# Kernel optimization log

Hardware: AMD Instinct MI355X
Metric: run time of the kernel (lower is better)

Reference implementation:

```python
import jax, jax.numpy as jnp
import numpy as np

B, T, E, H = 1024, 200, 128, 128
N_ITEMS, N_CATS = 100000, 1000
LN_EPS = 1e-5


def _prelu(x, a):
    return jnp.where(x >= 0, x, a * x)


def _layernorm(x, g, b):
    m = x.mean(-1, keepdims=True)
    v = ((x - m) ** 2).mean(-1, keepdims=True)
    return (x - m) / jnp.sqrt(v + LN_EPS) * g + b


def setup_inputs() -> dict:
    key = jax.random.key(0)
    it = iter(jax.random.split(key, 64))
    nx = lambda: next(it)
    def lin(out_d, in_d):
        s = 1.0 / np.sqrt(in_d)
        return jax.random.uniform(nx(), (out_d, in_d), jnp.float32, -s, s)
    inp = {}
    inp['behavior_ids'] = jax.random.randint(nx(), (B, T), 0, N_ITEMS)
    inp['candidate_id'] = jax.random.randint(nx(), (B,), 0, N_ITEMS)
    inp['candidate_cat'] = jax.random.randint(nx(), (B,), 0, N_CATS)
    inp['dense_features'] = jax.random.normal(nx(), (B, 5), jnp.float32)
    inp['item_emb'] = (jax.random.normal(nx(), (N_ITEMS, E), jnp.float32) * 0.01).at[0].set(0.0)
    inp['cat_emb'] = (jax.random.normal(nx(), (N_CATS, E // 2), jnp.float32) * 0.01).at[0].set(0.0)
    # nn.GRU params (gate order r,z,n)
    inp['gru_wih'] = lin(3 * H, E)
    inp['gru_whh'] = lin(3 * H, H)
    inp['gru_bih'] = jnp.zeros((3 * H,), jnp.float32)
    inp['gru_bhh'] = jnp.zeros((3 * H,), jnp.float32)
    # auxiliary_net: Linear(H,E) -> ReLU -> Linear(E,1)
    inp['aux_w1'] = lin(E, H); inp['aux_b1'] = jnp.zeros((E,), jnp.float32)
    inp['aux_w2'] = lin(1, E); inp['aux_b2'] = jnp.zeros((1,), jnp.float32)
    # attention_mlp: Linear(3H,64) -> PReLU -> Linear(64,1)
    inp['att_w1'] = lin(64, 3 * H); inp['att_b1'] = jnp.zeros((64,), jnp.float32)
    inp['att_a'] = jnp.array(0.25, jnp.float32)
    inp['att_w2'] = lin(1, 64); inp['att_b2'] = jnp.zeros((1,), jnp.float32)
    # AUGRU gates: Linear(2H, H) each
    inp['wz'] = lin(H, 2 * H); inp['bz'] = jnp.zeros((H,), jnp.float32)
    inp['wr'] = lin(H, 2 * H); inp['br'] = jnp.zeros((H,), jnp.float32)
    inp['wh'] = lin(H, 2 * H); inp['bh'] = jnp.zeros((H,), jnp.float32)
    # dense_proj Linear(5,32)
    inp['dp_w'] = lin(32, 5); inp['dp_b'] = jnp.zeros((32,), jnp.float32)
    # MLP: 352 -> 256 -> 128 -> 64, each Linear + LayerNorm + PReLU
    dims = [H + E + E // 2 + 32, 256, 128, 64]
    for i in range(3):
        inp[f'm_w{i+1}'] = lin(dims[i + 1], dims[i])
        inp[f'm_b{i+1}'] = jnp.zeros((dims[i + 1],), jnp.float32)
        inp[f'ln_g{i+1}'] = jnp.ones((dims[i + 1],), jnp.float32)
        inp[f'ln_b{i+1}'] = jnp.zeros((dims[i + 1],), jnp.float32)
        inp[f'pa{i+1}'] = jnp.array(0.25, jnp.float32)
    # 3 task heads Linear(64,1), stacked
    inp['heads_w'] = lin(3, 64); inp['heads_b'] = jnp.zeros((3,), jnp.float32)
    return inp


def _forward_core(behavior_ids, candidate_id, candidate_cat, dense_features,
                  item_emb, cat_emb, gru_wih, gru_whh, gru_bih, gru_bhh,
                  aux_w1, aux_b1, aux_w2, aux_b2,
                  att_w1, att_b1, att_a, att_w2, att_b2,
                  wz, bz, wr, br, wh, bh, dp_w, dp_b,
                  m_w1, m_b1, ln_g1, ln_b1, pa1,
                  m_w2, m_b2, ln_g2, ln_b2, pa2,
                  m_w3, m_b3, ln_g3, ln_b3, pa3,
                  heads_w, heads_b):
    beh = item_emb[behavior_ids]            # [B,T,E]
    cand = item_emb[candidate_id]           # [B,E]
    catv = cat_emb[candidate_cat]           # [B,E//2]
    Bsz = beh.shape[0]
    Hd = gru_whh.shape[1]
    h0 = jnp.zeros((Bsz, Hd), beh.dtype)
    # --- interest extractor GRU (cuDNN GRU math, gate order r,z,n) ---
    xp = jnp.einsum('bte,ge->btg', beh, gru_wih) + gru_bih  # [B,T,3H]
    def gru_step(h, x):
        hp = h @ gru_whh.T + gru_bhh
        xr, xz, xn = jnp.split(x, 3, -1)
        hr, hz, hn = jnp.split(hp, 3, -1)
        r = jax.nn.sigmoid(xr + hr)
        z = jax.nn.sigmoid(xz + hz)
        n = jnp.tanh(xn + r * hn)
        hnew = (1 - z) * n + z * h
        return hnew, hnew
    _, hs = jax.lax.scan(gru_step, h0, jnp.swapaxes(xp, 0, 1))
    hs = jnp.swapaxes(hs, 0, 1)             # [B,T,H]
    # --- auxiliary logits ---
    aux = jax.nn.relu(hs[:, :-1] @ aux_w1.T + aux_b1) @ aux_w2.T + aux_b2  # [B,T-1,1]
    # --- attention (embed_dim == hidden_size so cand_proj == candidate_emb) ---
    ce = cand[:, None, :]
    att_in = jnp.concatenate([hs, jnp.broadcast_to(ce, hs.shape), hs * ce], -1)  # [B,T,3H]
    scores = (_prelu(att_in @ att_w1.T + att_b1, att_a) @ att_w2.T + att_b2)[..., 0]
    att = jax.nn.softmax(scores, axis=-1)   # [B,T]
    # --- AUGRU: attention-modulated update gate ---
    def augru_step(h, xs):
        x, a = xs                           # x: [B,H], a: [B]
        comb = jnp.concatenate([x, h], -1)
        z = jax.nn.sigmoid(comb @ wz.T + bz)
        r = jax.nn.sigmoid(comb @ wr.T + br)
        comb_r = jnp.concatenate([x, r * h], -1)
        ht = jnp.tanh(comb_r @ wh.T + bh)
        zp = a[:, None] * z
        return (1 - zp) * h + zp * ht, None
    hT, _ = jax.lax.scan(augru_step, h0, (jnp.swapaxes(hs, 0, 1), att.T))
    # --- fusion MLP (dropout is identity in eval) ---
    dense_out = dense_features @ dp_w.T + dp_b
    x = jnp.concatenate([hT, cand, catv, dense_out], -1)  # [B,352]
    for (w, b, g, be, a) in ((m_w1, m_b1, ln_g1, ln_b1, pa1),
                             (m_w2, m_b2, ln_g2, ln_b2, pa2),
                             (m_w3, m_b3, ln_g3, ln_b3, pa3)):
        x = _prelu(_layernorm(x @ w.T + b, g, be), a)
    preds = jax.nn.sigmoid(x @ heads_w.T + heads_b)  # [B,3] == 3 heads of [B,1]
    return preds, aux


def reference(behavior_ids, candidate_id, candidate_cat, dense_features,
              item_emb, cat_emb, gru_wih, gru_whh, gru_bih, gru_bhh,
              aux_w1, aux_b1, aux_w2, aux_b2,
              att_w1, att_b1, att_a, att_w2, att_b2,
              wz, bz, wr, br, wh, bh, dp_w, dp_b,
              m_w1, m_b1, ln_g1, ln_b1, pa1,
              m_w2, m_b2, ln_g2, ln_b2, pa2,
              m_w3, m_b3, ln_g3, ln_b3, pa3,
              heads_w, heads_b):
    return _forward_core(behavior_ids, candidate_id, candidate_cat, dense_features,
                         item_emb, cat_emb, gru_wih, gru_whh, gru_bih, gru_bhh,
                         aux_w1, aux_b1, aux_w2, aux_b2,
                         att_w1, att_b1, att_a, att_w2, att_b2,
                         wz, bz, wr, br, wh, bh, dp_w, dp_b,
                         m_w1, m_b1, ln_g1, ln_b1, pa1,
                         m_w2, m_b2, ln_g2, ln_b2, pa2,
                         m_w3, m_b3, ln_g3, ln_b3, pa3,
                         heads_w, heads_b)
```

## Files before the change

kernel.cpp:

```cpp
#include <hip/hip_runtime.h>


typedef __bf16 bf16;
typedef float f32x4 __attribute__((ext_vector_type(4)));
typedef __bf16 bf16x8 __attribute__((ext_vector_type(8)));
typedef __bf16 bf16x4 __attribute__((ext_vector_type(4)));

#define MFMA16(a, b, c) __builtin_amdgcn_mfma_f32_16x16x32_bf16((a), (b), (c), 0, 0, 0)

#define BATCH 1024
#define SEQT 200
#define F32_ONE 0x3F800000u

__device__ __forceinline__ float sigm(float x) {
  return __builtin_amdgcn_rcpf(1.0f + __expf(-x));
}
__device__ __forceinline__ float tanh_fast(float x) {
  float ax = fabsf(x);
  float t = 1.0f - 2.0f * __builtin_amdgcn_rcpf(__expf(2.0f * ax) + 1.0f);
  return copysignf(t, x);
}

__device__ __forceinline__ void bar_lgkm() {
  asm volatile("s_waitcnt lgkmcnt(0)\n\ts_barrier" ::: "memory");
}

__device__ __forceinline__ void dma16(const void* g, void* l) {
  __builtin_amdgcn_global_load_lds((__attribute__((address_space(1))) void*)g,
                                   (__attribute__((address_space(3))) void*)l,
                                   16, 0, 0);
}

template <typename DT> __device__ __forceinline__ float ldf(const DT* p, long i);
template <> __device__ __forceinline__ float ldf<bf16>(const bf16* p, long i) { return (float)p[i]; }
template <> __device__ __forceinline__ float ldf<float>(const float* p, long i) { return p[i]; }

template <typename DT> __device__ __forceinline__ bf16x8 ld8(const DT* p, long i);
template <> __device__ __forceinline__ bf16x8 ld8<bf16>(const bf16* p, long i) {
  return *(const bf16x8*)(p + i);
}
template <> __device__ __forceinline__ bf16x8 ld8<float>(const float* p, long i) {
  f32x4 a = *(const f32x4*)(p + i);
  f32x4 b = *(const f32x4*)(p + i + 4);
  bf16x8 r;
  r[0] = (bf16)a[0]; r[1] = (bf16)a[1]; r[2] = (bf16)a[2]; r[3] = (bf16)a[3];
  r[4] = (bf16)b[0]; r[5] = (bf16)b[1]; r[6] = (bf16)b[2]; r[7] = (bf16)b[3];
  return r;
}

template <typename DT>
__device__ __forceinline__ void cast_body(const DT* __restrict__ src, bf16* __restrict__ dst) {
  const long i = ((long)blockIdx.x * 256 + threadIdx.x) * 8;
  if (i < 100000L * 128) *(bf16x8*)(dst + i) = ld8(src, i);
}
__global__ __launch_bounds__(256) void k_cast(
    const unsigned* __restrict__ disc, const void* src, bf16* dst) {
  if (*disc == F32_ONE) cast_body<float>((const float*)src, dst);
  else                  cast_body<bf16>((const bf16*)src, dst);
}

template <typename DT>
__device__ __forceinline__ void prep_body(
    const int* __restrict__ cid, const int* __restrict__ ccat,
    const DT* __restrict__ dense, const DT* __restrict__ item_emb,
    const DT* __restrict__ cat_emb, const DT* __restrict__ dp_w,
    const DT* __restrict__ dp_b, bf16* __restrict__ candbuf, bf16* __restrict__ xf) {
  const int b = blockIdx.x;
  const int t = threadIdx.x;
  bf16 v = (bf16)ldf(item_emb, (long)cid[b] * 128 + t);
  candbuf[b * 128 + t] = v;
  xf[(long)b * 352 + 128 + t] = v;
  if (t < 64) xf[(long)b * 352 + 256 + t] = (bf16)ldf(cat_emb, (long)ccat[b] * 64 + t);
  if (t < 32) {
    float s = ldf(dp_b, t);
    for (int k = 0; k < 5; k++) s += ldf(dense, b * 5 + k) * ldf(dp_w, t * 5 + k);
    xf[(long)b * 352 + 320 + t] = (bf16)s;
  }
}
__global__ __launch_bounds__(128) void k_prep(
    const unsigned* __restrict__ disc, const int* cid, const int* ccat,
    const void* dense, const void* item_emb, const void* cat_emb,
    const void* dp_w, const void* dp_b, bf16* candbuf, bf16* xf) {
  if (*disc == F32_ONE)
    prep_body<float>(cid, ccat, (const float*)dense, (const float*)item_emb,
                     (const float*)cat_emb, (const float*)dp_w, (const float*)dp_b, candbuf, xf);
  else
    prep_body<bf16>(cid, ccat, (const bf16*)dense, (const bf16*)item_emb,
                    (const bf16*)cat_emb, (const bf16*)dp_w, (const bf16*)dp_b, candbuf, xf);
}

template <typename DT>
__device__ __forceinline__ void gru5_body(
    const int* __restrict__ ids, const bf16* __restrict__ ieb,
    const DT* __restrict__ wih, const DT* __restrict__ whh,
    const DT* __restrict__ bih, const DT* __restrict__ bhh, bf16* __restrict__ hs,
    bf16 (*hA)[16][136], bf16 (*xb)[4][16][128]) {
  const int b0 = blockIdx.x * 16;
  const int tid = threadIdx.x;
  const int w = tid >> 6, lane = tid & 63, l15 = lane & 15, quad = lane >> 4;
  const int nc = w * 16 + l15;

  for (int i = tid; i < 2 * 16 * 136; i += 512) ((bf16*)hA)[i] = (bf16)0.0f;

  bf16x8 wir[4], wiz[4], win_[4], whr[4], whz[4], whn[4];
#pragma unroll
  for (int k = 0; k < 4; k++) {
    const long off = k * 32 + quad * 8;
    wir[k] = ld8(wih, (long)nc * 128 + off);
    wiz[k] = ld8(wih, (long)(128 + nc) * 128 + off);
    win_[k] = ld8(wih, (long)(256 + nc) * 128 + off);
    whr[k] = ld8(whh, (long)nc * 128 + off);
    whz[k] = ld8(whh, (long)(128 + nc) * 128 + off);
    whn[k] = ld8(whh, (long)(256 + nc) * 128 + off);
  }
  const float br_s = ldf(bih, nc) + ldf(bhh, nc);
  const float bz_s = ldf(bih, 128 + nc) + ldf(bhh, 128 + nc);
  const float bxn_s = ldf(bih, 256 + nc);
  const float bhn_s = ldf(bhh, 256 + nc);

  const int idrow = (tid >> 4) & 15;
  const int* idbase = ids + (long)(b0 + idrow) * SEQT;
  const int srcoff = ((tid & 15) ^ (idrow & 7)) * 8;

  auto DMA = [&](const int4 id4, int buf) {
#pragma unroll
    for (int j = 0; j < 2; j++) {
      const int slot = j * 2 + (tid >> 8);
      dma16(ieb + (long)((&id4.x)[slot]) * 128 + srcoff,
            (char*)&xb[buf][0][0][0] + (j * 512 + tid) * 16);
    }
  };

  const int srow = tid >> 5, sch = (tid & 31) * 4;
  bf16* hsb = hs + ((long)(b0 + srow) * SEQT) * 128 + sch;

  float hreg[4] = {0.f, 0.f, 0.f, 0.f};
  const f32x4 z4 = {0.f, 0.f, 0.f, 0.f};

  int4 idv = *(const int4*)(idbase);
  DMA(idv, 0);
  idv = *(const int4*)(idbase + 4);
  asm volatile("s_waitcnt vmcnt(1)" ::: "memory");
  __builtin_amdgcn_sched_barrier(0);
  __builtin_amdgcn_s_barrier();

#define GRU_STEP(P, S, WAITC)                                                  \
  {                                                                            \
    const int tt = t0 + (S);                                                   \
    bf16x8 af[4], xaf[4];                                                      \
    _Pragma("unroll") for (int k = 0; k < 4; k++) {                            \
      af[k] = *(const bf16x8*)&hA[P][l15][k * 32 + quad * 8];                  \
      xaf[k] = *(const bf16x8*)((const char*)&xb[buf][S][0][0] + l15 * 256 +   \
                                ((((k << 2) + quad) ^ (l15 & 7)) << 4));       \
    }                                                                          \
    { const int slot = tt ? tt - 1 : 0;                                        \
      bf16x4 hv = *(const bf16x4*)&hA[P][srow][sch];                           \
      *(bf16x4*)(hsb + (long)slot * 128) = hv; }                               \
    f32x4 ar = z4, az = z4, axn = z4, ahn = z4;                                \
    _Pragma("unroll") for (int k = 0; k < 4; k++) {                            \
      ar = MFMA16(xaf[k], wir[k], ar);                                         \
      az = MFMA16(xaf[k], wiz[k], az);                                         \
      axn = MFMA16(xaf[k], win_[k], axn);                                      \
    }                                                                          \
    _Pragma("unroll") for (int k = 0; k < 4; k++) {                            \
      ar = MFMA16(af[k], whr[k], ar);                                          \
      az = MFMA16(af[k], whz[k], az);                                          \
      ahn = MFMA16(af[k], whn[k], ahn);                                        \
    }                                                                          \
    _Pragma("unroll") for (int r = 0; r < 4; r++) {                            \
      float r_ = sigm(ar[r] + br_s);                                           \
      float z_ = sigm(az[r] + bz_s);                                           \
      float n_ = tanh_fast(axn[r] + bxn_s + r_ * (ahn[r] + bhn_s));            \
      float hnew = (1.0f - z_) * n_ + z_ * hreg[r];                            \
      hreg[r] = hnew;                                                          \
      hA[(P) ^ 1][quad * 4 + r][nc] = (bf16)hnew;                              \
    }                                                                          \
    if (WAITC) {                                                               \
       \
      asm volatile("s_waitcnt vmcnt(5) lgkmcnt(0)\n\ts_barrier" ::: "memory"); \
    } else {                                                                   \
      bar_lgkm();                                                              \
    }                                                                          \
  }

  for (int c = 0; c < 50; c++) {
    const int t0 = c * 4;
    const int buf = c & 1;
    if (c < 49) {
      DMA(idv, buf ^ 1);
      int nid = (c + 2) * 4; if (nid > 196) nid = 196;
      idv = *(const int4*)(idbase + nid);
    }
    GRU_STEP(0, 0, 0) GRU_STEP(1, 1, 0) GRU_STEP(0, 2, 0) GRU_STEP(1, 3, (c < 49))
  }
#undef GRU_STEP
  { bf16x4 hv = *(const bf16x4*)&hA[0][srow][sch];
    *(bf16x4*)(hsb + (long)(SEQT - 1) * 128) = hv; }
}
__global__ __launch_bounds__(512, 1) void k_gru5(
    const unsigned* __restrict__ disc, const int* ids, const bf16* ieb,
    const void* wih, const void* whh, const void* bih, const void* bhh, bf16* hs) {
  __shared__ __align__(16) bf16 hA[2][16][136];
  __shared__ __align__(16) bf16 xb[2][4][16][128];
  if (*disc == F32_ONE)
    gru5_body<float>(ids, ieb, (const float*)wih, (const float*)whh,
                     (const float*)bih, (const float*)bhh, hs, hA, xb);
  else
    gru5_body<bf16>(ids, ieb, (const bf16*)wih, (const bf16*)whh,
                    (const bf16*)bih, (const bf16*)bhh, hs, hA, xb);
}

template <typename DT>
__device__ __forceinline__ void attaux_body(
    const bf16* __restrict__ hs, const int* __restrict__ cid,
    const DT* __restrict__ item_emb,
    const DT* __restrict__ aw1, const DT* __restrict__ ab1,
    const DT* __restrict__ aw2, const DT* __restrict__ ab2,
    const DT* __restrict__ tw1, const DT* __restrict__ tb1, const DT* __restrict__ ta,
    const DT* __restrict__ tw2, const DT* __restrict__ tb2,
    float* __restrict__ sc, float* __restrict__ outaux,
    bf16 (*As)[64][128], float (*scPt)[64], float (*scPa)[64]) {
  const int t0 = blockIdx.x * 64;
  const int b0 = blockIdx.y * 16;
  const int tid = threadIdx.x, w = tid >> 6, lane = tid & 63, l15 = lane & 15, quad = lane >> 4;

  const int tn = w * 16 + l15;
  bf16x8 wth[4], wtc[4], wthc[4], wa0[4], wa1[4];
#pragma unroll
  for (int k = 0; k < 4; k++) {
    const long off = k * 32 + quad * 8;
    wth[k]  = ld8(tw1, (long)tn * 384 + off);
    wtc[k]  = ld8(tw1, (long)tn * 384 + 128 + off);
    wthc[k] = ld8(tw1, (long)tn * 384 + 256 + off);
    wa0[k]  = ld8(aw1, (long)((2 * w) * 16 + l15) * 128 + off);
    wa1[k]  = ld8(aw1, (long)((2 * w + 1) * 16 + l15) * 128 + off);
  }
  const float tb1c = ldf(tb1, tn), tw2c = ldf(tw2, tn);
  const float ab1c0 = ldf(ab1, (2 * w) * 16 + l15), aw2c0 = ldf(aw2, (2 * w) * 16 + l15);
  const float ab1c1 = ldf(ab1, (2 * w + 1) * 16 + l15), aw2c1 = ldf(aw2, (2 * w + 1) * 16 + l15);
  const float aP = ldf(ta, 0), tb2s = ldf(tb2, 0), ab2s = ldf(ab2, 0);

  auto DMA = [&](int b, int buf) {
#pragma unroll
    for (int c = 0; c < 4; c++) {
      const int idx = c * 256 + tid;
      const int row = idx >> 4, p = idx & 15;
      int t = t0 + row; if (t > SEQT - 1) t = SEQT - 1;
      const bf16* src = hs + ((long)b * SEQT + t) * 128 + ((p ^ (row & 7)) * 8);
      dma16(src, (char*)(&As[buf][0][0]) + idx * 16);
    }
  };
  auto CANDLD = [&](int b, bf16x8* cf) {
#pragma unroll
    for (int k = 0; k < 4; k++)
      cf[k] = ld8(item_emb, (long)cid[b] * 128 + k * 32 + quad * 8);
  };

  const f32x4 z4 = {0.f, 0.f, 0.f, 0.f};
  bf16x8 candA[4], candB[4];
  DMA(b0, 0);
  CANDLD(b0, candA);
  asm volatile("s_waitcnt vmcnt(0)" ::: "memory");
  __builtin_amdgcn_sched_barrier(0);
  __builtin_amdgcn_s_barrier();

#define AA_STEP(BI, CUSE, CPF)                                                 \
  {                                                                            \
    const int b = b0 + (BI);                                                   \
    const int buf = (BI) & 1;                                                  \
    if ((BI) + 1 < 16) { DMA(b + 1, buf ^ 1); CANDLD(b + 1, CPF); }            \
    _Pragma("unroll") for (int m = 0; m < 4; m++) {                            \
      const bf16* arow = &As[buf][m * 16 + l15][0];                            \
      bf16x8 af[4], hcf[4];                                                    \
      _Pragma("unroll") for (int k = 0; k < 4; k++)                            \
        af[k] = *(const bf16x8*)((const char*)arow +                           \
                                 (((k * 4 + quad) ^ (l15 & 7)) << 4));         \
      _Pragma("unroll") for (int k = 0; k < 4; k++)                            \
      _Pragma("unroll") for (int j = 0; j < 8; j++)                            \
        hcf[k][j] = (bf16)((float)af[k][j] * (float)CUSE[k][j]);               \
      f32x4 at = z4, aa0 = z4, aa1 = z4;                                       \
      _Pragma("unroll") for (int k = 0; k < 4; k++) {                          \
        at = MFMA16(af[k], wth[k], at);                                        \
        at = MFMA16(CUSE[k], wtc[k], at);                                      \
        at = MFMA16(hcf[k], wthc[k], at);                                      \
        aa0 = MFMA16(af[k], wa0[k], aa0);                                      \
        aa1 = MFMA16(af[k], wa1[k], aa1);                                      \
      }                                                                        \
      float tp[4], ap[4];                                                      \
      _Pragma("unroll") for (int r = 0; r < 4; r++) {                          \
        float y = at[r] + tb1c;                                                \
        y = (y >= 0.f) ? y : aP * y;                                           \
        tp[r] = y * tw2c;                                                      \
        float y0 = aa0[r] + ab1c0;                                             \
        float y1 = aa1[r] + ab1c1;                                             \
        ap[r] = (y0 > 0.f ? y0 : 0.f) * aw2c0 + (y1 > 0.f ? y1 : 0.f) * aw2c1; \
      }                                                                        \
      _Pragma("unroll") for (int mm = 1; mm < 16; mm <<= 1)                    \
      _Pragma("unroll") for (int r = 0; r < 4; r++) {                          \
        tp[r] += __shfl_xor(tp[r], mm, 64);                                    \
        ap[r] += __shfl_xor(ap[r], mm, 64);                                    \
      }                                                                        \
      if (l15 == 0) {                                                          \
        *(float4*)&scPt[w][m * 16 + quad * 4] =                                \
            make_float4(tp[0], tp[1], tp[2], tp[3]);                           \
        *(float4*)&scPa[w][m * 16 + quad * 4] =                                \
            make_float4(ap[0], ap[1], ap[2], ap[3]);                           \
      }                                                                        \
    }                                                                          \
    bar_lgkm();                                                                \
    if (tid < 64) {                                                            \
      int t = t0 + tid;                                                        \
      if (t < SEQT) {                                                          \
        float s = scPt[0][tid] + scPt[1][tid] + scPt[2][tid] + scPt[3][tid];   \
        sc[(long)b * SEQT + t] = s + tb2s;                                     \
      }                                                                        \
    } else if (tid < 128) {                                                    \
      int tt2 = tid - 64, t = t0 + tt2;                                        \
      if (t < SEQT - 1) {                                                      \
        float s = scPa[0][tt2] + scPa[1][tt2] + scPa[2][tt2] + scPa[3][tt2];   \
        outaux[(long)b * 199 + t] = s + ab2s;                                  \
      }                                                                        \
    }                                                                          \
    asm volatile("s_waitcnt vmcnt(0) lgkmcnt(0)" ::: "memory");                \
    __builtin_amdgcn_sched_barrier(0);                                         \
    __builtin_amdgcn_s_barrier();                                              \
  }

  for (int bi = 0; bi < 16; bi += 2) {
    AA_STEP(bi, candA, candB)
    AA_STEP(bi + 1, candB, candA)
  }
#undef AA_STEP
}
__global__ __launch_bounds__(256, 1) void k_attaux(
    const unsigned* __restrict__ disc, const bf16* hs, const int* cid,
    const void* item_emb,
    const void* aw1, const void* ab1, const void* aw2, const void* ab2,
    const void* tw1, const void* tb1, const void* ta, const void* tw2, const void* tb2,
    float* sc, float* outaux) {
  __shared__ __align__(16) bf16 As[2][64][128];
  __shared__ __align__(16) float scPt[4][64];
  __shared__ __align__(16) float scPa[4][64];
  if (*disc == F32_ONE)
    attaux_body<float>(hs, cid, (const float*)item_emb,
                       (const float*)aw1, (const float*)ab1, (const float*)aw2, (const float*)ab2,
                       (const float*)tw1, (const float*)tb1, (const float*)ta,
                       (const float*)tw2, (const float*)tb2, sc, outaux, As, scPt, scPa);
  else
    attaux_body<bf16>(hs, cid, (const bf16*)item_emb,
                      (const bf16*)aw1, (const bf16*)ab1, (const bf16*)aw2, (const bf16*)ab2,
                      (const bf16*)tw1, (const bf16*)tb1, (const bf16*)ta,
                      (const bf16*)tw2, (const bf16*)tb2, sc, outaux, As, scPt, scPa);
}

__global__ __launch_bounds__(256) void k_softmax(float* __restrict__ sc) {
  const int b = blockIdx.x, tid = threadIdx.x;
  __shared__ float red[256];
  float v = (tid < SEQT) ? sc[(long)b * SEQT + tid] : -1e30f;
  red[tid] = v; __syncthreads();
  for (int s = 128; s > 0; s >>= 1) { if (tid < s) red[tid] = fmaxf(red[tid], red[tid + s]); __syncthreads(); }
  float mx = red[0]; __syncthreads();
  float e = (tid < SEQT) ? __expf(v - mx) : 0.f;
  red[tid] = e; __syncthreads();
  for (int s = 128; s > 0; s >>= 1) { if (tid < s) red[tid] += red[tid + s]; __syncthreads(); }
  float inv = 1.0f / red[0];
  if (tid < SEQT) sc[(long)b * SEQT + tid] = e * inv;
}

template <typename DT>
__device__ __forceinline__ void augru5_body(
    const bf16* __restrict__ hsrc, const float* __restrict__ att,
    const DT* __restrict__ wz, const DT* __restrict__ wr, const DT* __restrict__ wh,
    const DT* __restrict__ bzv, const DT* __restrict__ brv, const DT* __restrict__ bhv,
    bf16* __restrict__ xf_out,
    bf16 (*hA)[16][136], bf16 (*rhA)[136], float (*attL)[201],
    bf16 (*xb)[4][16][128]) {
  const int b0 = blockIdx.x * 16;
  const int tid = threadIdx.x;
  const int w = tid >> 6, lane = tid & 63, l15 = lane & 15, quad = lane >> 4;
  const int nc = w * 16 + l15;

  for (int i = tid; i < 2 * 16 * 136; i += 512) ((bf16*)hA)[i] = (bf16)0.0f;
  for (int i = tid; i < 16 * SEQT; i += 512) {
    int r = i / SEQT, c = i - r * SEQT;
    attL[r][c] = att[(long)(b0 + r) * SEQT + c];
  }

  bf16x8 wzx[4], wzh[4], wrx[4], wrh[4], whx[4], whh_[4];
#pragma unroll
  for (int k = 0; k < 4; k++) {
    const long off = k * 32 + quad * 8;
    wzx[k] = ld8(wz, (long)nc * 256 + off);
    wzh[k] = ld8(wz, (long)nc * 256 + 128 + off);
    wrx[k] = ld8(wr, (long)nc * 256 + off);
    wrh[k] = ld8(wr, (long)nc * 256 + 128 + off);
    whx[k] = ld8(wh, (long)nc * 256 + off);
    whh_[k] = ld8(wh, (long)nc * 256 + 128 + off);
  }
  const float bz_s = ldf(bzv, nc);
  const float br_s = ldf(brv, nc);
  const float bh_s = ldf(bhv, nc);

  const int drow = (tid >> 4) & 15;
  const int srcoff = ((tid & 15) ^ (drow & 7)) * 8;
  auto DMA = [&](int t0, int buf) {
#pragma unroll
    for (int j = 0; j < 2; j++) {
      const int slot = j * 2 + (tid >> 8);
      dma16(hsrc + ((long)(b0 + drow) * SEQT + t0 + slot) * 128 + srcoff,
            (char*)&xb[buf][0][0][0] + (j * 512 + tid) * 16);
    }
  };

  float hreg[4] = {0.f, 0.f, 0.f, 0.f};
  const f32x4 z4 = {0.f, 0.f, 0.f, 0.f};

  DMA(0, 0);
  asm volatile("s_waitcnt vmcnt(0)" ::: "memory");
  __builtin_amdgcn_sched_barrier(0);
  __builtin_amdgcn_s_barrier();

#define AUGRU_STEP(P, S, WAITC)                                                \
  {                                                                            \
    const int tt = t0 + (S);                                                   \
    bf16x8 af[4], xaf[4];                                                      \
    _Pragma("unroll") for (int k = 0; k < 4; k++) {                            \
      af[k] = *(const bf16x8*)&hA[P][l15][k * 32 + quad * 8];                  \
      xaf[k] = *(const bf16x8*)((const char*)&xb[buf][S][0][0] + l15 * 256 +   \
                                ((((k << 2) + quad) ^ (l15 & 7)) << 4));       \
    }                                                                          \
    f32x4 az = z4, ar = z4, axh = z4;                                          \
    _Pragma("unroll") for (int k = 0; k < 4; k++) {                            \
      az = MFMA16(xaf[k], wzx[k], az);                                         \
      ar = MFMA16(xaf[k], wrx[k], ar);                                         \
      axh = MFMA16(xaf[k], whx[k], axh);                                       \
    }                                                                          \
    _Pragma("unroll") for (int k = 0; k < 4; k++) {                            \
      az = MFMA16(af[k], wzh[k], az);                                          \
      ar = MFMA16(af[k], wrh[k], ar);                                          \
    }                                                                          \
    float zp[4];                                                               \
    _Pragma("unroll") for (int r = 0; r < 4; r++) {                            \
      float a_ = attL[quad * 4 + r][tt];                                       \
      float z_ = sigm(az[r] + bz_s);                                           \
      float r_ = sigm(ar[r] + br_s);                                           \
      zp[r] = a_ * z_;                                                         \
      rhA[quad * 4 + r][nc] = (bf16)(r_ * hreg[r]);                            \
    }                                                                          \
    bar_lgkm();                                                                \
    bf16x8 rf[4];                                                              \
    _Pragma("unroll") for (int k = 0; k < 4; k++)                              \
      rf[k] = *(const bf16x8*)&rhA[l15][k * 32 + quad * 8];                    \
    f32x4 ahh = axh;                                                           \
    _Pragma("unroll") for (int k = 0; k < 4; k++)                              \
      ahh = MFMA16(rf[k], whh_[k], ahh);                                       \
    _Pragma("unroll") for (int r = 0; r < 4; r++) {                            \
      float ht = tanh_fast(ahh[r] + bh_s);                                     \
      float hnew = (1.f - zp[r]) * hreg[r] + zp[r] * ht;                       \
      hreg[r] = hnew;                                                          \
      hA[(P) ^ 1][quad * 4 + r][nc] = (bf16)hnew;                              \
    }                                                                          \
    if (WAITC) {                                                               \
                     \
      asm volatile("s_waitcnt vmcnt(0) lgkmcnt(0)\n\ts_barrier" ::: "memory"); \
    } else {                                                                   \
      bar_lgkm();                                                              \
    }                                                                          \
  }

  for (int c = 0; c < 50; c++) {
    const int t0 = c * 4;
    const int buf = c & 1;
    if (c < 49) DMA((c + 1) * 4, buf ^ 1);
    AUGRU_STEP(0, 0, 0) AUGRU_STEP(1, 1, 0) AUGRU_STEP(0, 2, 0) AUGRU_STEP(1, 3, (c < 49))
  }
#undef AUGRU_STEP
#pragma unroll
  for (int r = 0; r < 4; r++)
    xf_out[(long)(b0 + quad * 4 + r) * 352 + nc] = (bf16)hreg[r];
}
__global__ __launch_bounds__(512, 1) void k_augru5(
    const unsigned* __restrict__ disc, const bf16* hsrc, const float* att,
    const void* wz, const void* wr, const void* wh,
    const void* bzv, const void* brv, const void* bhv, bf16* xf_out) {
  __shared__ __align__(16) bf16 hA[2][16][136];
  __shared__ __align__(16) bf16 rhA[16][136];
  __shared__ __align__(16) float attL[16][201];
  __shared__ __align__(16) bf16 xb[2][4][16][128];
  if (*disc == F32_ONE)
    augru5_body<float>(hsrc, att, (const float*)wz, (const float*)wr, (const float*)wh,
                       (const float*)bzv, (const float*)brv, (const float*)bhv, xf_out,
                       hA, rhA, attL, xb);
  else
    augru5_body<bf16>(hsrc, att, (const bf16*)wz, (const bf16*)wr, (const bf16*)wh,
                      (const bf16*)bzv, (const bf16*)brv, (const bf16*)bhv, xf_out,
                      hA, rhA, attL, xb);
}

template <typename DT>
__device__ __forceinline__ void mlp_body(
    const bf16* __restrict__ xf,
    const DT* __restrict__ w1, const DT* __restrict__ b1, const DT* __restrict__ g1, const DT* __restrict__ be1, const DT* __restrict__ pa1,
    const DT* __restrict__ w2, const DT* __restrict__ b2, const DT* __restrict__ g2, const DT* __restrict__ be2, const DT* __restrict__ pa2,
    const DT* __restrict__ w3, const DT* __restrict__ b3, const DT* __restrict__ g3, const DT* __restrict__ be3, const DT* __restrict__ pa3,
    const DT* __restrict__ hw, const DT* __restrict__ hb, float* __restrict__ preds,
    float (*xs)[352], float (*ys)[256]) {
  const int tid = threadIdx.x, w = tid >> 6, lane = tid & 63;
  const int b = blockIdx.x * 4 + w;
  for (int i = lane; i < 352; i += 64) xs[w][i] = (float)xf[(long)b * 352 + i];
  __syncthreads();
  float acc1[4];
#pragma unroll
  for (int oi = 0; oi < 4; oi++) {
    int o = lane + 64 * oi;
    float s = ldf(b1, o);
    for (int k = 0; k < 352; k += 8) {
      bf16x8 wv = ld8(w1, (long)o * 352 + k);
#pragma unroll
      for (int j = 0; j < 8; j++) s += xs[w][k + j] * (float)wv[j];
    }
    acc1[oi] = s;
  }
  float sm = acc1[0] + acc1[1] + acc1[2] + acc1[3];
#pragma unroll
  for (int m = 1; m < 64; m <<= 1) sm += __shfl_xor(sm, m, 64);
  float mean = sm * (1.0f / 256.0f);
  float vs = 0.f;
#pragma unroll
  for (int oi = 0; oi < 4; oi++) { float d = acc1[oi] - mean; vs += d * d; }
#pragma unroll
  for (int m = 1; m < 64; m <<= 1) vs += __shfl_xor(vs, m, 64);
  float rstd = rsqrtf(vs * (1.0f / 256.0f) + 1e-5f);
  float a1 = ldf(pa1, 0);
#pragma unroll
  for (int oi = 0; oi < 4; oi++) {
    int o = lane + 64 * oi;
    float y = (acc1[oi] - mean) * rstd * ldf(g1, o) + ldf(be1, o);
    ys[w][o] = (y >= 0.f) ? y : a1 * y;
  }
  __syncthreads();
  float acc2[2];
#pragma unroll
  for (int oi = 0; oi < 2; oi++) {
    int o = lane + 64 * oi;
    float s = ldf(b2, o);
    for (int k = 0; k < 256; k += 8) {
      bf16x8 wv = ld8(w2, (long)o * 256 + k);
#pragma unroll
      for (int j = 0; j < 8; j++) s += ys[w][k + j] * (float)wv[j];
    }
    acc2[oi] = s;
  }
  sm = acc2[0] + acc2[1];
#pragma unroll
  for (int m = 1; m < 64; m <<= 1) sm += __shfl_xor(sm, m, 64);
  mean = sm * (1.0f / 128.0f);
  vs = 0.f;
#pragma unroll
  for (int oi = 0; oi < 2; oi++) { float d = acc2[oi] - mean; vs += d * d; }
#pragma unroll
  for (int m = 1; m < 64; m <<= 1) vs += __shfl_xor(vs, m, 64);
  rstd = rsqrtf(vs * (1.0f / 128.0f) + 1e-5f);
  float a2 = ldf(pa2, 0);
  __syncthreads();
#pragma unroll
  for (int oi = 0; oi < 2; oi++) {
    int o = lane + 64 * oi;
    float y = (acc2[oi] - mean) * rstd * ldf(g2, o) + ldf(be2, o);
    xs[w][o] = (y >= 0.f) ? y : a2 * y;
  }
  __syncthreads();
  float s3 = ldf(b3, lane);
  for (int k = 0; k < 128; k += 8) {
    bf16x8 wv = ld8(w3, (long)lane * 128 + k);
#pragma unroll
    for (int j = 0; j < 8; j++) s3 += xs[w][k + j] * (float)wv[j];
  }
  sm = s3;
#pragma unroll
  for (int m = 1; m < 64; m <<= 1) sm += __shfl_xor(sm, m, 64);
  mean = sm * (1.0f / 64.0f);
  float d3 = s3 - mean;
  vs = d3 * d3;
#pragma unroll
  for (int m = 1; m < 64; m <<= 1) vs += __shfl_xor(vs, m, 64);
  rstd = rsqrtf(vs * (1.0f / 64.0f) + 1e-5f);
  float a3 = ldf(pa3, 0);
  float y3 = d3 * rstd * ldf(g3, lane) + ldf(be3, lane);
  y3 = (y3 >= 0.f) ? y3 : a3 * y3;
  ys[w][lane] = y3;
  __syncthreads();
  if (lane < 3) {
    float s = ldf(hb, lane);
    for (int k = 0; k < 64; k++) s += ys[w][k] * ldf(hw, lane * 64 + k);
    preds[(long)b * 3 + lane] = sigm(s);
  }
}
__global__ __launch_bounds__(256) void k_mlp(
    const unsigned* __restrict__ disc, const bf16* xf,
    const void* w1, const void* b1, const void* g1, const void* be1, const void* pa1,
    const void* w2, const void* b2, const void* g2, const void* be2, const void* pa2,
    const void* w3, const void* b3, const void* g3, const void* be3, const void* pa3,
    const void* hw, const void* hb, float* preds) {
  __shared__ float xs[4][352];
  __shared__ float ys[4][256];
  if (*disc == F32_ONE)
    mlp_body<float>(xf,
        (const float*)w1, (const float*)b1, (const float*)g1, (const float*)be1, (const float*)pa1,
        (const float*)w2, (const float*)b2, (const float*)g2, (const float*)be2, (const float*)pa2,
        (const float*)w3, (const float*)b3, (const float*)g3, (const float*)be3, (const float*)pa3,
        (const float*)hw, (const float*)hb, preds, xs, ys);
  else
    mlp_body<bf16>(xf,
        (const bf16*)w1, (const bf16*)b1, (const bf16*)g1, (const bf16*)be1, (const bf16*)pa1,
        (const bf16*)w2, (const bf16*)b2, (const bf16*)g2, (const bf16*)be2, (const bf16*)pa2,
        (const bf16*)w3, (const bf16*)b3, (const bf16*)g3, (const bf16*)be3, (const bf16*)pa3,
        (const bf16*)hw, (const bf16*)hb, preds, xs, ys);
}

extern "C" void kernel_launch(void* const* d_in, const int* in_sizes, int n_in,
                              void* d_out, int out_size, void* d_ws, size_t ws_size,
                              hipStream_t stream) {
  const int* behavior_ids = (const int*)d_in[0];
  const int* candidate_id = (const int*)d_in[1];
  const int* candidate_cat = (const int*)d_in[2];
  const void* dense = d_in[3];
  const void* item_emb = d_in[4];
  const void* cat_emb = d_in[5];
  const void* gru_wih = d_in[6];
  const void* gru_whh = d_in[7];
  const void* gru_bih = d_in[8];
  const void* gru_bhh = d_in[9];
  const void* aux_w1 = d_in[10];
  const void* aux_b1 = d_in[11];
  const void* aux_w2 = d_in[12];
  const void* aux_b2 = d_in[13];
  const void* att_w1 = d_in[14];
  const void* att_b1 = d_in[15];
  const void* att_a = d_in[16];
  const void* att_w2 = d_in[17];
  const void* att_b2 = d_in[18];
  const void* wz = d_in[19];
  const void* bz = d_in[20];
  const void* wr = d_in[21];
  const void* br = d_in[22];
  const void* wh = d_in[23];
  const void* bh = d_in[24];
  const void* dp_w = d_in[25];
  const void* dp_b = d_in[26];
  const void* m_w1 = d_in[27];
  const void* m_b1 = d_in[28];
  const void* ln_g1 = d_in[29];
  const void* ln_b1 = d_in[30];
  const void* pa1 = d_in[31];
  const void* m_w2 = d_in[32];
  const void* m_b2 = d_in[33];
  const void* ln_g2 = d_in[34];
  const void* ln_b2 = d_in[35];
  const void* pa2 = d_in[36];
  const void* m_w3 = d_in[37];
  const void* m_b3 = d_in[38];
  const void* ln_g3 = d_in[39];
  const void* ln_b3 = d_in[40];
  const void* pa3 = d_in[41];
  const void* heads_w = d_in[42];
  const void* heads_b = d_in[43];
  (void)in_sizes; (void)n_in; (void)out_size; (void)ws_size;

  const unsigned* disc = (const unsigned*)ln_g1;

  char* ws = (char*)d_ws;
  bf16* HS = (bf16*)(ws);
  float* SC = (float*)(ws + 52428800L);
  bf16* CAND = (bf16*)(ws + 53248000L);
  bf16* XF = (bf16*)(ws + 53510144L);
  bf16* IEB = (bf16*)(ws + 54231040L);
  float* OUT = (float*)d_out;

  k_cast<<<6250, 256, 0, stream>>>(disc, item_emb, IEB);
  k_prep<<<BATCH, 128, 0, stream>>>(disc, candidate_id, candidate_cat, dense, item_emb,
                                    cat_emb, dp_w, dp_b, CAND, XF);
  k_gru5<<<64, 512, 0, stream>>>(disc, behavior_ids, IEB, gru_wih, gru_whh,
                                 gru_bih, gru_bhh, HS);
  k_attaux<<<dim3(4, 64), 256, 0, stream>>>(disc, HS, candidate_id, item_emb,
                                            aux_w1, aux_b1, aux_w2, aux_b2,
                                            att_w1, att_b1, att_a, att_w2, att_b2,
                                            SC, OUT + 3072);
  k_softmax<<<BATCH, 256, 0, stream>>>(SC);
  k_augru5<<<64, 512, 0, stream>>>(disc, HS, SC, wz, wr, wh, bz, br, bh, XF);
  k_mlp<<<256, 256, 0, stream>>>(disc, XF,
      m_w1, m_b1, ln_g1, ln_b1, pa1,
      m_w2, m_b2, ln_g2, ln_b2, pa2,
      m_w3, m_b3, ln_g3, ln_b3, pa3,
      heads_w, heads_b, OUT);
}
```

Measured before the change: 733.9 us.

## Fuse softmax into AUGRU, fold prep into MLP, relax attaux barrier waits

Removes the standalone softmax kernel by computing the per-row softmax over attention scores inside the AUGRU kernel after loading them to shared memory, using wavefront shuffles. Removes the prep kernel by gathering candidate embedding, category embedding and dense projection directly in the MLP kernel. Changes the hidden-state LDS row padding from 136 to 132, and lets the attaux loop wait for only part of its outstanding loads before the barrier instead of all of them. This cuts two launches and some global round-trips. The partial vmcnt wait relies on correct load counting, and the new padding may change LDS bank conflicts.

```diff
diff --git a/kernel.cpp b/kernel.cpp
--- a/kernel.cpp
+++ b/kernel.cpp
@@ -11,6 +11,7 @@
 #define BATCH 1024
 #define SEQT 200
 #define F32_ONE 0x3F800000u
+#define HPAD 132
 
 __device__ __forceinline__ float sigm(float x) {
   return __builtin_amdgcn_rcpf(1.0f + __expf(-x));
@@ -53,54 +54,24 @@
   const long i = ((long)blockIdx.x * 256 + threadIdx.x) * 8;
   if (i < 100000L * 128) *(bf16x8*)(dst + i) = ld8(src, i);
 }
-__global__ __launch_bounds__(256) void k_cast(
+__global__ __launch_bounds__(256) void k_init(
     const unsigned* __restrict__ disc, const void* src, bf16* dst) {
   if (*disc == F32_ONE) cast_body<float>((const float*)src, dst);
   else                  cast_body<bf16>((const bf16*)src, dst);
 }
 
 template <typename DT>
-__device__ __forceinline__ void prep_body(
-    const int* __restrict__ cid, const int* __restrict__ ccat,
-    const DT* __restrict__ dense, const DT* __restrict__ item_emb,
-    const DT* __restrict__ cat_emb, const DT* __restrict__ dp_w,
-    const DT* __restrict__ dp_b, bf16* __restrict__ candbuf, bf16* __restrict__ xf) {
-  const int b = blockIdx.x;
-  const int t = threadIdx.x;
-  bf16 v = (bf16)ldf(item_emb, (long)cid[b] * 128 + t);
-  candbuf[b * 128 + t] = v;
-  xf[(long)b * 352 + 128 + t] = v;
-  if (t < 64) xf[(long)b * 352 + 256 + t] = (bf16)ldf(cat_emb, (long)ccat[b] * 64 + t);
-  if (t < 32) {
-    float s = ldf(dp_b, t);
-    for (int k = 0; k < 5; k++) s += ldf(dense, b * 5 + k) * ldf(dp_w, t * 5 + k);
-    xf[(long)b * 352 + 320 + t] = (bf16)s;
-  }
-}
-__global__ __launch_bounds__(128) void k_prep(
-    const unsigned* __restrict__ disc, const int* cid, const int* ccat,
-    const void* dense, const void* item_emb, const void* cat_emb,
-    const void* dp_w, const void* dp_b, bf16* candbuf, bf16* xf) {
-  if (*disc == F32_ONE)
-    prep_body<float>(cid, ccat, (const float*)dense, (const float*)item_emb,
-                     (const float*)cat_emb, (const float*)dp_w, (const float*)dp_b, candbuf, xf);
-  else
-    prep_body<bf16>(cid, ccat, (const bf16*)dense, (const bf16*)item_emb,
-                    (const bf16*)cat_emb, (const bf16*)dp_w, (const bf16*)dp_b, candbuf, xf);
-}
-
-template <typename DT>
-__device__ __forceinline__ void gru5_body(
+__device__ __forceinline__ void gru_body(
     const int* __restrict__ ids, const bf16* __restrict__ ieb,
     const DT* __restrict__ wih, const DT* __restrict__ whh,
     const DT* __restrict__ bih, const DT* __restrict__ bhh, bf16* __restrict__ hs,
-    bf16 (*hA)[16][136], bf16 (*xb)[4][16][128]) {
+    bf16 (*hA)[16][HPAD], bf16 (*xb)[4][16][128]) {
   const int b0 = blockIdx.x * 16;
   const int tid = threadIdx.x;
   const int w = tid >> 6, lane = tid & 63, l15 = lane & 15, quad = lane >> 4;
   const int nc = w * 16 + l15;
 
-  for (int i = tid; i < 2 * 16 * 136; i += 512) ((bf16*)hA)[i] = (bf16)0.0f;
+  for (int i = tid; i < 2 * 16 * HPAD; i += 512) ((bf16*)hA)[i] = (bf16)0.0f;
 
   bf16x8 wir[4], wiz[4], win_[4], whr[4], whz[4], whn[4];
 #pragma unroll
@@ -118,9 +89,9 @@
   const float bxn_s = ldf(bih, 256 + nc);
   const float bhn_s = ldf(bhh, 256 + nc);
 
-  const int idrow = (tid >> 4) & 15;
-  const int* idbase = ids + (long)(b0 + idrow) * SEQT;
-  const int srcoff = ((tid & 15) ^ (idrow & 7)) * 8;
+  const int drow = (tid >> 4) & 15;
+  const int* idbase = ids + (long)(b0 + drow) * SEQT;
+  const int srcoff = ((tid & 15) ^ (drow & 7)) * 8;
 
   auto DMA = [&](const int4 id4, int buf) {
 #pragma unroll
@@ -197,17 +168,17 @@
   { bf16x4 hv = *(const bf16x4*)&hA[0][srow][sch];
     *(bf16x4*)(hsb + (long)(SEQT - 1) * 128) = hv; }
 }
-__global__ __launch_bounds__(512, 1) void k_gru5(
+__global__ __launch_bounds__(512, 1) void k_gru(
     const unsigned* __restrict__ disc, const int* ids, const bf16* ieb,
     const void* wih, const void* whh, const void* bih, const void* bhh, bf16* hs) {
-  __shared__ __align__(16) bf16 hA[2][16][136];
+  __shared__ __align__(16) bf16 hA[2][16][HPAD];
   __shared__ __align__(16) bf16 xb[2][4][16][128];
   if (*disc == F32_ONE)
-    gru5_body<float>(ids, ieb, (const float*)wih, (const float*)whh,
-                     (const float*)bih, (const float*)bhh, hs, hA, xb);
+    gru_body<float>(ids, ieb, (const float*)wih, (const float*)whh,
+                    (const float*)bih, (const float*)bhh, hs, hA, xb);
   else
-    gru5_body<bf16>(ids, ieb, (const bf16*)wih, (const bf16*)whh,
-                    (const bf16*)bih, (const bf16*)bhh, hs, hA, xb);
+    gru_body<bf16>(ids, ieb, (const bf16*)wih, (const bf16*)whh,
+                   (const bf16*)bih, (const bf16*)bhh, hs, hA, xb);
 }
 
 template <typename DT>
@@ -321,9 +292,12 @@
         outaux[(long)b * 199 + t] = s + ab2s;                                  \
       }                                                                        \
     }                                                                          \
-    asm volatile("s_waitcnt vmcnt(0) lgkmcnt(0)" ::: "memory");                \
-    __builtin_amdgcn_sched_barrier(0);                                         \
-    __builtin_amdgcn_s_barrier();                                              \
+    if ((BI) + 1 < 16) {                                                       \
+             \
+      asm volatile("s_waitcnt vmcnt(4) lgkmcnt(0)\n\ts_barrier" ::: "memory"); \
+    } else {                                                                   \
+      asm volatile("s_waitcnt vmcnt(0) lgkmcnt(0)\n\ts_barrier" ::: "memory"); \
+    }                                                                          \
   }
 
   for (int bi = 0; bi < 16; bi += 2) {
@@ -353,37 +327,38 @@
                       (const bf16*)tw2, (const bf16*)tb2, sc, outaux, As, scPt, scPa);
 }
 
-__global__ __launch_bounds__(256) void k_softmax(float* __restrict__ sc) {
-  const int b = blockIdx.x, tid = threadIdx.x;
-  __shared__ float red[256];
-  float v = (tid < SEQT) ? sc[(long)b * SEQT + tid] : -1e30f;
-  red[tid] = v; __syncthreads();
-  for (int s = 128; s > 0; s >>= 1) { if (tid < s) red[tid] = fmaxf(red[tid], red[tid + s]); __syncthreads(); }
-  float mx = red[0]; __syncthreads();
-  float e = (tid < SEQT) ? __expf(v - mx) : 0.f;
-  red[tid] = e; __syncthreads();
-  for (int s = 128; s > 0; s >>= 1) { if (tid < s) red[tid] += red[tid + s]; __syncthreads(); }
-  float inv = 1.0f / red[0];
-  if (tid < SEQT) sc[(long)b * SEQT + tid] = e * inv;
-}
-
 template <typename DT>
-__device__ __forceinline__ void augru5_body(
+__device__ __forceinline__ void augru_body(
     const bf16* __restrict__ hsrc, const float* __restrict__ att,
     const DT* __restrict__ wz, const DT* __restrict__ wr, const DT* __restrict__ wh,
     const DT* __restrict__ bzv, const DT* __restrict__ brv, const DT* __restrict__ bhv,
     bf16* __restrict__ xf_out,
-    bf16 (*hA)[16][136], bf16 (*rhA)[136], float (*attL)[201],
+    bf16 (*hA)[16][HPAD], bf16 (*rhA)[HPAD], float (*attL)[201],
     bf16 (*xb)[4][16][128]) {
   const int b0 = blockIdx.x * 16;
   const int tid = threadIdx.x;
   const int w = tid >> 6, lane = tid & 63, l15 = lane & 15, quad = lane >> 4;
   const int nc = w * 16 + l15;
 
-  for (int i = tid; i < 2 * 16 * 136; i += 512) ((bf16*)hA)[i] = (bf16)0.0f;
+  for (int i = tid; i < 2 * 16 * HPAD; i += 512) ((bf16*)hA)[i] = (bf16)0.0f;
   for (int i = tid; i < 16 * SEQT; i += 512) {
     int r = i / SEQT, c = i - r * SEQT;
     attL[r][c] = att[(long)(b0 + r) * SEQT + c];
+  }
+  bar_lgkm();
+  {
+    const int row = tid >> 5, lt = tid & 31;
+    float mx = -1e30f;
+    for (int t = lt; t < SEQT; t += 32) mx = fmaxf(mx, attL[row][t]);
+#pragma unroll
+    for (int m = 1; m < 32; m <<= 1) mx = fmaxf(mx, __shfl_xor(mx, m, 64));
+    float sum = 0.f;
+    for (int t = lt; t < SEQT; t += 32) sum += __expf(attL[row][t] - mx);
+#pragma unroll
+    for (int m = 1; m < 32; m <<= 1) sum += __shfl_xor(sum, m, 64);
+    float inv = __builtin_amdgcn_rcpf(sum);
+    for (int t = lt; t < SEQT; t += 32)
+      attL[row][t] = __expf(attL[row][t] - mx) * inv;
   }
 
   bf16x8 wzx[4], wzh[4], wrx[4], wrh[4], whx[4], whh_[4];
@@ -416,7 +391,7 @@
   const f32x4 z4 = {0.f, 0.f, 0.f, 0.f};
 
   DMA(0, 0);
-  asm volatile("s_waitcnt vmcnt(0)" ::: "memory");
+  asm volatile("s_waitcnt vmcnt(0) lgkmcnt(0)" ::: "memory");
   __builtin_amdgcn_sched_barrier(0);
   __builtin_amdgcn_s_barrier();
 
@@ -479,27 +454,30 @@
   for (int r = 0; r < 4; r++)
     xf_out[(long)(b0 + quad * 4 + r) * 352 + nc] = (bf16)hreg[r];
 }
-__global__ __launch_bounds__(512, 1) void k_augru5(
+__global__ __launch_bounds__(512, 1) void k_augru(
     const unsigned* __restrict__ disc, const bf16* hsrc, const float* att,
     const void* wz, const void* wr, const void* wh,
     const void* bzv, const void* brv, const void* bhv, bf16* xf_out) {
-  __shared__ __align__(16) bf16 hA[2][16][136];
-  __shared__ __align__(16) bf16 rhA[16][136];
+  __shared__ __align__(16) bf16 hA[2][16][HPAD];
+  __shared__ __align__(16) bf16 rhA[16][HPAD];
   __shared__ __align__(16) float attL[16][201];
   __shared__ __align__(16) bf16 xb[2][4][16][128];
   if (*disc == F32_ONE)
-    augru5_body<float>(hsrc, att, (const float*)wz, (const float*)wr, (const float*)wh,
-                       (const float*)bzv, (const float*)brv, (const float*)bhv, xf_out,
-                       hA, rhA, attL, xb);
+    augru_body<float>(hsrc, att, (const float*)wz, (const float*)wr, (const float*)wh,
+                      (const float*)bzv, (const float*)brv, (const float*)bhv, xf_out,
+                      hA, rhA, attL, xb);
   else
-    augru5_body<bf16>(hsrc, att, (const bf16*)wz, (const bf16*)wr, (const bf16*)wh,
-                      (const bf16*)bzv, (const bf16*)brv, (const bf16*)bhv, xf_out,
-                      hA, rhA, attL, xb);
+    augru_body<bf16>(hsrc, att, (const bf16*)wz, (const bf16*)wr, (const bf16*)wh,
+                     (const bf16*)bzv, (const bf16*)brv, (const bf16*)bhv, xf_out,
+                     hA, rhA, attL, xb);
 }
 
 template <typename DT>
 __device__ __forceinline__ void mlp_body(
     const bf16* __restrict__ xf,
+    const int* __restrict__ cid, const int* __restrict__ ccat,
+    const DT* __restrict__ dense, const DT* __restrict__ item_emb,
+    const DT* __restrict__ cat_emb, const DT* __restrict__ dp_w, const DT* __restrict__ dp_b,
     const DT* __restrict__ w1, const DT* __restrict__ b1, const DT* __restrict__ g1, const DT* __restrict__ be1, const DT* __restrict__ pa1,
     const DT* __restrict__ w2, const DT* __restrict__ b2, const DT* __restrict__ g2, const DT* __restrict__ be2, const DT* __restrict__ pa2,
     const DT* __restrict__ w3, const DT* __restrict__ b3, const DT* __restrict__ g3, const DT* __restrict__ be3, const DT* __restrict__ pa3,
@@ -507,7 +485,16 @@
     float (*xs)[352], float (*ys)[256]) {
   const int tid = threadIdx.x, w = tid >> 6, lane = tid & 63;
   const int b = blockIdx.x * 4 + w;
-  for (int i = lane; i < 352; i += 64) xs[w][i] = (float)xf[(long)b * 352 + i];
+  for (int i = lane; i < 128; i += 64) {
+    xs[w][i] = (float)xf[(long)b * 352 + i];
+    xs[w][128 + i] = ldf(item_emb, (long)cid[b] * 128 + i);
+  }
+  if (lane < 64) xs[w][256 + lane] = ldf(cat_emb, (long)ccat[b] * 64 + lane);
+  if (lane < 32) {
+    float s = ldf(dp_b, lane);
+    for (int k = 0; k < 5; k++) s += ldf(dense, b * 5 + k) * ldf(dp_w, lane * 5 + k);
+    xs[w][320 + lane] = s;
+  }
   __syncthreads();
   float acc1[4];
 #pragma unroll
@@ -598,6 +585,8 @@
 }
 __global__ __launch_bounds__(256) void k_mlp(
     const unsigned* __restrict__ disc, const bf16* xf,
+    const int* cid, const int* ccat, const void* dense, const void* item_emb,
+    const void* cat_emb, const void* dp_w, const void* dp_b,
     const void* w1, const void* b1, const void* g1, const void* be1, const void* pa1,
     const void* w2, const void* b2, const void* g2, const void* be2, const void* pa2,
     const void* w3, const void* b3, const void* g3, const void* be3, const void* pa3,
@@ -605,13 +594,15 @@
   __shared__ float xs[4][352];
   __shared__ float ys[4][256];
   if (*disc == F32_ONE)
-    mlp_body<float>(xf,
+    mlp_body<float>(xf, cid, ccat, (const float*)dense, (const float*)item_emb,
+        (const float*)cat_emb, (const float*)dp_w, (const float*)dp_b,
         (const float*)w1, (const float*)b1, (const float*)g1, (const float*)be1, (const float*)pa1,
         (const float*)w2, (const float*)b2, (const float*)g2, (const float*)be2, (const float*)pa2,
         (const float*)w3, (const float*)b3, (const float*)g3, (const float*)be3, (const float*)pa3,
         (const float*)hw, (const float*)hb, preds, xs, ys);
   else
-    mlp_body<bf16>(xf,
+    mlp_body<bf16>(xf, cid, ccat, (const bf16*)dense, (const bf16*)item_emb,
+        (const bf16*)cat_emb, (const bf16*)dp_w, (const bf16*)dp_b,
         (const bf16*)w1, (const bf16*)b1, (const bf16*)g1, (const bf16*)be1, (const bf16*)pa1,
         (const bf16*)w2, (const bf16*)b2, (const bf16*)g2, (const bf16*)be2, (const bf16*)pa2,
         (const bf16*)w3, (const bf16*)b3, (const bf16*)g3, (const bf16*)be3, (const bf16*)pa3,
@@ -672,23 +663,20 @@
   char* ws = (char*)d_ws;
   bf16* HS = (bf16*)(ws);
   float* SC = (float*)(ws + 52428800L);
-  bf16* CAND = (bf16*)(ws + 53248000L);
   bf16* XF = (bf16*)(ws + 53510144L);
   bf16* IEB = (bf16*)(ws + 54231040L);
   float* OUT = (float*)d_out;
 
-  k_cast<<<6250, 256, 0, stream>>>(disc, item_emb, IEB);
-  k_prep<<<BATCH, 128, 0, stream>>>(disc, candidate_id, candidate_cat, dense, item_emb,
-                                    cat_emb, dp_w, dp_b, CAND, XF);
-  k_gru5<<<64, 512, 0, stream>>>(disc, behavior_ids, IEB, gru_wih, gru_whh,
-                                 gru_bih, gru_bhh, HS);
+  k_init<<<6250, 256, 0, stream>>>(disc, item_emb, IEB);
+  k_gru<<<64, 512, 0, stream>>>(disc, behavior_ids, IEB, gru_wih, gru_whh,
+                                gru_bih, gru_bhh, HS);
   k_attaux<<<dim3(4, 64), 256, 0, stream>>>(disc, HS, candidate_id, item_emb,
                                             aux_w1, aux_b1, aux_w2, aux_b2,
                                             att_w1, att_b1, att_a, att_w2, att_b2,
                                             SC, OUT + 3072);
-  k_softmax<<<BATCH, 256, 0, stream>>>(SC);
-  k_augru5<<<64, 512, 0, stream>>>(disc, HS, SC, wz, wr, wh, bz, br, bh, XF);
+  k_augru<<<64, 512, 0, stream>>>(disc, HS, SC, wz, wr, wh, bz, br, bh, XF);
   k_mlp<<<256, 256, 0, stream>>>(disc, XF,
+      candidate_id, candidate_cat, dense, item_emb, cat_emb, dp_w, dp_b,
       m_w1, m_b1, ln_g1, ln_b1, pa1,
       m_w2, m_b2, ln_g2, ln_b2, pa2,
       m_w3, m_b3, ln_g3, ln_b3, pa3,
```

Result: slower. 1.091 ms (+48.7%).
